# Optimization experiments

Hardware: AMD Instinct MI355X
Metric: run time of the kernel (lower is better)

Reference implementation:

```python
import jax, jax.numpy as jnp
import numpy as np

NUM_CLASSES = 2


def setup_inputs() -> dict:
    key = jax.random.key(0)
    k1, k2, k3 = jax.random.split(key, 3)
    query_features = jax.random.normal(k1, (16384, 2048), dtype=jnp.float32)
    support_features = jax.random.normal(k2, (2048, 2048), dtype=jnp.float32)
    support_labels = jax.random.randint(k3, (2048,), 0, NUM_CLASSES, dtype=jnp.int32)
    return {
        "query_features": query_features,
        "support_features": support_features,
        "support_labels": support_labels,
    }


def _cov(x):
    # unbiased covariance over rows (observations), columns are variables
    xc = x - jnp.mean(x, axis=0, keepdims=True)
    return (xc.T @ xc) / (x.shape[0] - 1)


def _class_stats(features, labels, c):
    # masked per-class mean + unbiased covariance (masked rows contribute 0)
    mask = (labels == c).astype(features.dtype)  # [S]
    n_c = jnp.sum(mask)
    mean_c = (mask @ features) / n_c  # [D]
    xc = (features - mean_c) * mask[:, None]  # [S, D]
    cov_c = (xc.T @ xc) / (n_c - 1.0)  # [D, D]
    return mean_c, cov_c, n_c


def reference(query_features, support_features, support_labels):
    D = support_features.shape[1]
    task_cov = _cov(support_features)  # [D, D]
    eye = jnp.eye(D, dtype=support_features.dtype)

    def per_class(c):
        mean_c, cov_c, n_c = _class_stats(support_features, support_labels, c)
        lam = jnp.minimum(n_c / (n_c + 1.0), 0.1)
        prec = jnp.linalg.inv(lam * cov_c + (1.0 - lam) * task_cov + 0.1 * eye)
        return mean_c, prec

    means, precisions = jax.vmap(per_class)(jnp.arange(NUM_CLASSES))  # [C,D], [C,D,D]

    # Mahalanobis quadratic form: logits[n,c] = -(mu_c - q_n)^T P_c (mu_c - q_n)
    diff = means[:, None, :] - query_features[None, :, :]  # [C, N, D]
    first_half = jnp.einsum("cnd,cde->cne", diff, precisions)  # [C, N, D]
    logits = -jnp.sum(first_half * diff, axis=2).T  # [N, C]
    return logits
```

## Files before the change

kernel.cpp:

```cpp
#include <hip/hip_runtime.h>

#define D   2048
#define S   2048
#define NQ  16384
#define DD  ((long)D * (long)D)

#define IDX_N      0
#define IDX_NORMS  16
#define IDX_S      48
#define IDX_SUM    256
#define IDX_MU     4608
#define IDX_MUF    8704
#define IDX_U      10752
#define IDX_V      14848
#define IDX_W2     18944
#define IDX_ACC    32768
#define SMALL_FLOATS 65536

#define NPOW 8
#define NNS  3

typedef unsigned short u16;
typedef __attribute__((ext_vector_type(8))) short short8;
typedef __attribute__((ext_vector_type(4))) short short4v;
typedef __attribute__((ext_vector_type(4))) float f32x4;

__device__ __forceinline__ u16 f2bf(float f) {
    unsigned u = __float_as_uint(f);
    u += 0x7fff + ((u >> 16) & 1);
    return (u16)(u >> 16);
}

__device__ __forceinline__ float bf2f(u16 b) {
    return __uint_as_float(((unsigned)b) << 16);
}

__device__ __forceinline__ void gl16(const void* g, void* l) {
    __builtin_amdgcn_global_load_lds((const __attribute__((address_space(1))) void*)g,
                                     (__attribute__((address_space(3))) void*)l, 16, 0, 0);
}


__global__ void k_counts(const int* __restrict__ lab, float* __restrict__ W) {
    int c0 = 0, c1 = 0;
    for (int i = threadIdx.x; i < S; i += 256) {
        int l = lab[i];
        c0 += (l == 0);
        c1 += (l == 1);
    }
    atomicAdd(&W[IDX_N + 0], (float)c0);
    atomicAdd(&W[IDX_N + 1], (float)c1);
}

__global__ void k_colsums(const float* __restrict__ X, const int* __restrict__ lab,
                          float* __restrict__ W) {
    int d  = blockIdx.x * 256 + threadIdx.x;
    int i0 = blockIdx.y * 128;
    float s0 = 0.f, s1 = 0.f;
    for (int i = i0; i < i0 + 128; ++i) {
        float v = X[(long)i * D + d];
        int   l = lab[i];
        s0 += (l == 0) ? v : 0.f;
        s1 += (l == 1) ? v : 0.f;
    }
    atomicAdd(&W[IDX_SUM + d],     s0);
    atomicAdd(&W[IDX_SUM + D + d], s1);
}

__global__ void k_stats(float* __restrict__ W) {
    int d = blockIdx.x * 256 + threadIdx.x;
    float n0 = W[IDX_N], n1 = W[IDX_N + 1];
    float s0 = W[IDX_SUM + d], s1 = W[IDX_SUM + D + d];
    W[IDX_MU + d]     = s0 / n0;
    W[IDX_MU + D + d] = s1 / n1;
    W[IDX_MUF + d]    = (s0 + s1) / (float)S;
    unsigned h = (unsigned)d * 2654435761u;
    float r = 0.5f + (float)((h >> 16) & 1023) / 1024.f;
    W[IDX_V + d]     = r;
    W[IDX_V + D + d] = r;
}

__global__ void k_build_M(const float* __restrict__ G, const float* __restrict__ W,
                          u16* __restrict__ Mp) {
    long idx = (long)blockIdx.x * 256 + threadIdx.x;
    int d = (int)(idx / D), e = (int)(idx % D);
    float n0 = W[IDX_N], n1 = W[IDX_N + 1];
    float mufd = W[IDX_MUF + d],     mufe = W[IDX_MUF + e];
    float m0d  = W[IDX_MU + d],      m0e  = W[IDX_MU + e];
    float m1d  = W[IDX_MU + D + d],  m1e  = W[IDX_MU + D + e];
    float a0 = G[idx], a1 = G[DD + idx];
    float task = (a0 + a1 - (float)S * mufd * mufe) * (1.f / (float)(S - 1));
    float c0 = (a0 - n0 * m0d * m0e) / (n0 - 1.f);
    float c1 = (a1 - n1 * m1d * m1e) / (n1 - 1.f);
    float l0 = fminf(n0 / (n0 + 1.f), 0.1f);
    float l1 = fminf(n1 / (n1 + 1.f), 0.1f);
    float eye = (d == e) ? 0.1f : 0.f;
    long po = ((long)(d >> 3) * D + e) * 8 + (d & 7);
    Mp[po]      = f2bf(l0 * c0 + (1.f - l0) * task + eye);
    Mp[DD + po] = f2bf(l1 * c1 + (1.f - l1) * task + eye);
}

__global__ void k_pow(const u16* __restrict__ Mp, float* __restrict__ W, int it) {
    int z = blockIdx.y;
    const u16* Mz = Mp + (long)z * DD;
    float* V  = W + IDX_V  + z * D;
    float* W2 = W + IDX_W2 + z * D;
    const float* in = (it & 1) ? W2 : V;
    float*       out = (it & 1) ? V  : W2;
    float sc = (it > 0) ? rsqrtf(W[IDX_NORMS + z * 16 + it - 1]) : 1.f;
    __shared__ float sin_[D];
    __shared__ float part[8][32];
    for (int e = threadIdx.x; e < D; e += 256) sin_[e] = in[e] * sc;
    __syncthreads();
    int col = blockIdx.x * 32 + (threadIdx.x & 31);
    int sl  = threadIdx.x >> 5;
    float p = 0.f;
    for (int g = sl * 32; g < sl * 32 + 32; ++g) {
        short8 mv = *(const short8*)&Mz[((long)g * D + col) * 8];
#pragma unroll
        for (int j = 0; j < 8; ++j)
            p = fmaf(bf2f((u16)mv[j]), sin_[g * 8 + j], p);
    }
    part[sl][threadIdx.x & 31] = p;
    __syncthreads();
    if (threadIdx.x < 32) {
        float w = 0.f;
#pragma unroll
        for (int s = 0; s < 8; ++s) w += part[s][threadIdx.x];
        out[col] = w;
        float q = w * w;
#pragma unroll
        for (int off = 16; off; off >>= 1) q += __shfl_down(q, off, 32);
        if (threadIdx.x == 0) atomicAdd(&W[IDX_NORMS + z * 16 + it], q);
    }
}

__global__ void k_matvec_u(const u16* __restrict__ Pp, float* __restrict__ W) {
    int z = blockIdx.y;
    const u16* Pz = Pp + (long)z * DD;
    __shared__ float smu[D];
    __shared__ float part[8][32];
    for (int e = threadIdx.x; e < D; e += 256) smu[e] = W[IDX_MU + z * D + e];
    __syncthreads();
    int col = blockIdx.x * 32 + (threadIdx.x & 31);
    int sl  = threadIdx.x >> 5;
    float p = 0.f;
    for (int g = sl * 32; g < sl * 32 + 32; ++g) {
        short8 mv = *(const short8*)&Pz[((long)g * D + col) * 8];
#pragma unroll
        for (int j = 0; j < 8; ++j)
            p = fmaf(bf2f((u16)mv[j]), smu[g * 8 + j], p);
    }
    part[sl][threadIdx.x & 31] = p;
    __syncthreads();
    if (threadIdx.x < 32) {
        float w = 0.f;
#pragma unroll
        for (int s = 0; s < 8; ++s) w += part[s][threadIdx.x];
        W[IDX_U + z * D + col] = w;
    }
}

__global__ void k_dot(float* __restrict__ W) {
    int z = blockIdx.x;
    float t = 0.f;
    for (int d = threadIdx.x; d < D; d += 256)
        t += W[IDX_MU + z * D + d] * W[IDX_U + z * D + d];
    for (int off = 32; off; off >>= 1) t += __shfl_down(t, off);
    __shared__ float sm[4];
    int wv = threadIdx.x >> 6, ln = threadIdx.x & 63;
    if (ln == 0) sm[wv] = t;
    __syncthreads();
    if (threadIdx.x == 0) W[IDX_S + z] = sm[0] + sm[1] + sm[2] + sm[3];
}

__global__ void k_finalize(const float* __restrict__ W, float* __restrict__ out) {
    int idx = blockIdx.x * 256 + threadIdx.x;
    int z = idx & 1;
    out[idx] = -(W[IDX_ACC + idx] + W[IDX_S + z]);
}


__global__ void k_pack_S(const float* __restrict__ Xs, const int* __restrict__ lab,
                         u16* __restrict__ Sp, u16* __restrict__ S01p) {
    int d = blockIdx.x * 256 + threadIdx.x;
    int a = blockIdx.y;
    short8 p, p0, p1;
#pragma unroll
    for (int j = 0; j < 8; ++j) {
        int i = a * 8 + j;
        float v = Xs[(long)i * D + d];
        int   l = lab[i];
        short b = (short)f2bf(v);
        p[j]  = b;
        p0[j] = (l == 0) ? b : (short)0;
        p1[j] = (l == 1) ? b : (short)0;
    }
    long off = ((long)a * D + d) * 8;
    *(short8*)&Sp[off]        = p;
    *(short8*)&S01p[off]      = p0;
    *(short8*)&S01p[DD + off] = p1;
}

#define TLS 520
__global__ void k_pack_Q(const float* __restrict__ Q, u16* __restrict__ Qp) {
    __shared__ u16 tl[32 * TLS];
    int m0 = blockIdx.x * 64;
    int f0 = blockIdx.y * 256;
    int t = threadIdx.x;
#pragma unroll
    for (int p = 0; p < 16; ++p) {
        int idx = p * 256 + t;
        int r  = idx >> 6;
        int c4 = idx & 63;
        float4 v = *(const float4*)&Q[(long)(m0 + r) * D + f0 + c4 * 4];
        u16* dst = &tl[(c4 >> 1) * TLS + r * 8 + (c4 & 1) * 4];
        dst[0] = f2bf(v.x); dst[1] = f2bf(v.y);
        dst[2] = f2bf(v.z); dst[3] = f2bf(v.w);
    }
    __syncthreads();
#pragma unroll
    for (int p = 0; p < 8; ++p) {
        int idx = p * 256 + t;
        int g = idx >> 6;
        int r = idx & 63;
        short8 pk = *(const short8*)&tl[g * TLS + r * 8];
        *(short8*)&Qp[((long)(f0 / 8 + g) * NQ + m0 + r) * 8] = pk;
    }
}

__global__ void __launch_bounds__(512)
bgemmQ(const u16* __restrict__ Ap, const u16* __restrict__ Bp,
       long sA, long sB, int lda, int K,
       const float* __restrict__ u, float* __restrict__ acc2) {
    int z = blockIdx.z;
    const u16* A = Ap + z * sA;
    const u16* B = Bp + z * sB;

    int nwg = gridDim.x * gridDim.y;
    int id  = blockIdx.y * gridDim.x + blockIdx.x;
    int cpx = nwg >> 3;
    int swz = (id & 7) * cpx + (id >> 3);
    int bx = swz % gridDim.x, by = swz / gridDim.x;

    int n0 = bx * 256;
    int m0 = by * 256;
    int tid = threadIdx.x;
    int w = tid >> 6, lane = tid & 63;
    int wr = w >> 2, wc = w & 3;
    int lhi = lane >> 4, llo = lane & 15;

    __shared__ short lds[65536];

    f32x4 acc[8][4];
#pragma unroll
    for (int i = 0; i < 8; ++i)
#pragma unroll
        for (int j = 0; j < 4; ++j) acc[i][j] = (f32x4)(0.f);

    auto stage = [&](int H) {
        char* ldsB = (char*)lds + (H & 3) * 32768;
#pragma unroll
        for (int q = 0; q < 4; ++q) {
            int id4  = w * 4 + q;
            int isB  = id4 >> 4;
            int kg   = (id4 >> 2) & 3;
            int colq = id4 & 3;
            long row = (long)(4 * H + kg);
            const u16* src = isB ? (B + (row * (long)D   + n0 + colq * 64) * 8)
                                 : (A + (row * (long)lda + m0 + colq * 64) * 8);
            gl16((const char*)src + lane * 16,
                 ldsB + isB * 16384 + kg * 4096 + colq * 1024);
        }
    };

    auto compute = [&](int h) {
        const short* As = lds + (h & 3) * 16384 + lhi * 2048;
        const short* Bs = As + 8192;
        short8 af[8], bfr[4];
#pragma unroll
        for (int i = 0; i < 8; ++i)
            af[i] = *(const short8*)&As[(wr * 128 + i * 16 + llo) * 8];
#pragma unroll
        for (int j = 0; j < 4; ++j)
            bfr[j] = *(const short8*)&Bs[(wc * 64 + j * 16 + llo) * 8];
        __builtin_amdgcn_s_setprio(1);
#pragma unroll
        for (int i = 0; i < 8; ++i)
#pragma unroll
            for (int j = 0; j < 4; ++j)
                acc[i][j] = __builtin_amdgcn_mfma_f32_16x16x32_bf16(af[i], bfr[j], acc[i][j], 0, 0, 0);
        __builtin_amdgcn_s_setprio(0);
    };

    const int NH = K >> 5;
    stage(0); stage(1); stage(2);
    for (int h = 0; h <= NH - 3; ++h) {
        asm volatile("s_waitcnt vmcnt(8)" ::: "memory");
        asm volatile("s_barrier" ::: "memory");
        if (h < NH - 3) stage(h + 3);
        compute(h);
    }
    asm volatile("s_waitcnt vmcnt(4)" ::: "memory");
    asm volatile("s_barrier" ::: "memory");
    compute(NH - 2);
    asm volatile("s_waitcnt vmcnt(0)" ::: "memory");
    asm volatile("s_barrier" ::: "memory");
    compute(NH - 1);

    float uv[4];
#pragma unroll
    for (int j = 0; j < 4; ++j) uv[j] = u[z * D + n0 + wc * 64 + j * 16 + llo];
#pragma unroll
    for (int i = 0; i < 8; ++i) {
#pragma unroll
        for (int r = 0; r < 4; ++r) {
            int row = m0 + wr * 128 + i * 16 + lhi * 4 + r;
            float t = 0.f;
#pragma unroll
            for (int j = 0; j < 4; ++j) {
                int n = n0 + wc * 64 + j * 16 + llo;
                float qv = bf2f(A[((long)(n >> 3) * NQ + row) * 8 + (n & 7)]);
                t += (acc[i][j][r] - 2.f * uv[j]) * qv;
            }
            t += __shfl_xor(t, 1);
            t += __shfl_xor(t, 2);
            t += __shfl_xor(t, 4);
            t += __shfl_xor(t, 8);
            if (llo == 0) atomicAdd(&acc2[row * 2 + z], t);
        }
    }
}

template <int EPI>
__global__ void __launch_bounds__(512)
bgemmD(const u16* __restrict__ Ap, const u16* __restrict__ Bp,
       float* __restrict__ Cf, u16* __restrict__ Cp,
       u16* __restrict__ Cp2, const u16* __restrict__ Ep,
       long sA, long sB, long sCf, long sCp,
       int lda, int K,
       const float* __restrict__ u) {
    int z = blockIdx.z;
    const u16* A = Ap + z * sA;
    const u16* B = Bp + z * sB;

    int nwg = gridDim.x * gridDim.y;
    int id  = blockIdx.y * gridDim.x + blockIdx.x;
    int cpx = nwg >> 3;
    int swz = (id & 7) * cpx + (id >> 3);
    int bx = swz % gridDim.x, by = swz / gridDim.x;

    int n0 = bx * 256;
    int m0 = by * 128;
    int tid = threadIdx.x;
    int w = tid >> 6, lane = tid & 63;
    int wr = w >> 2, wc = w & 3;
    int lhi = lane >> 4, llo = lane & 15;

    __shared__ short lds[73728];

    f32x4 acc[4][4];
#pragma unroll
    for (int i = 0; i < 4; ++i)
#pragma unroll
        for (int j = 0; j < 4; ++j) acc[i][j] = (f32x4)(0.f);

    auto stage = [&](int H, int sl) {
        char* ldsB = (char*)lds + sl * 49152;
#pragma unroll
        for (int q = 0; q < 6; ++q) {
            int idq  = w * 6 + q;
            bool isB = idq >= 16;
            int idr  = isB ? idq - 16 : idq;
            int kg   = isB ? (idr >> 2) : (idr >> 1);
            int colq = isB ? (idr & 3)  : (idr & 1);
            long row = (long)(8 * H + kg);
            const u16* src = isB ? (B + (row * (long)D   + n0 + colq * 64) * 8)
                                 : (A + (row * (long)lda + m0 + colq * 64) * 8);
            char* dst = ldsB + (isB ? (16384 + kg * 4096 + colq * 1024)
                                    : (kg * 2048 + colq * 1024));
            gl16((const char*)src + lane * 16, dst);
        }
    };

    auto compute = [&](int h, int sl) {
        const short* slot = lds + sl * 24576;
#pragma unroll
        for (int kk = 0; kk < 2; ++kk) {
            const short* As = slot + (kk * 4 + lhi) * 1024;
            const short* Bs = slot + 8192 + (kk * 4 + lhi) * 2048;
            short8 af[4], bfr[4];
#pragma unroll
            for (int i = 0; i < 4; ++i)
                af[i] = *(const short8*)&As[(wr * 64 + i * 16 + llo) * 8];
#pragma unroll
            for (int j = 0; j < 4; ++j)
                bfr[j] = *(const short8*)&Bs[(wc * 64 + j * 16 + llo) * 8];
            __builtin_amdgcn_s_setprio(1);
#pragma unroll
            for (int i = 0; i < 4; ++i)
#pragma unroll
                for (int j = 0; j < 4; ++j)
                    acc[i][j] = __builtin_amdgcn_mfma_f32_16x16x32_bf16(af[i], bfr[j], acc[i][j], 0, 0, 0);
            __builtin_amdgcn_s_setprio(0);
        }
    };

    const int NH = K >> 6;
    stage(0, 0); stage(1, 1);
    int sl = 0;
    for (int h = 0; h <= NH - 3; ++h) {
        asm volatile("s_waitcnt vmcnt(6)" ::: "memory");
        asm volatile("s_barrier" ::: "memory");
        int sl2 = (sl == 0) ? 2 : sl - 1;
        stage(h + 2, sl2);
        compute(h, sl);
        sl = (sl == 2) ? 0 : sl + 1;
    }
    asm volatile("s_waitcnt vmcnt(6)" ::: "memory");
    asm volatile("s_barrier" ::: "memory");
    compute(NH - 2, sl);
    sl = (sl == 2) ? 0 : sl + 1;
    asm volatile("s_waitcnt vmcnt(0)" ::: "memory");
    asm volatile("s_barrier" ::: "memory");
    compute(NH - 1, sl);

    if (EPI == 0) {
        float* C = Cf + z * sCf;
#pragma unroll
        for (int i = 0; i < 4; ++i) {
            int m_b = m0 + wr * 64 + i * 16 + lhi * 4;
#pragma unroll
            for (int j = 0; j < 4; ++j) {
                int n = n0 + wc * 64 + j * 16 + llo;
#pragma unroll
                for (int r = 0; r < 4; ++r)
                    C[(long)(m_b + r) * D + n] = acc[i][j][r];
            }
        }
    } else if (EPI == 1) {
        u16* P = Cp + z * sCp;
#pragma unroll
        for (int i = 0; i < 4; ++i) {
            int m_b = m0 + wr * 64 + i * 16 + lhi * 4;
#pragma unroll
            for (int j = 0; j < 4; ++j) {
                int n = n0 + wc * 64 + j * 16 + llo;
                short4v pk;
#pragma unroll
                for (int r = 0; r < 4; ++r) {
                    float v = ((m_b + r) == n ? 1.f : 0.f) - acc[i][j][r];
                    pk[r] = (short)f2bf(v);
                }
                *(short4v*)((char*)P + ((long)((m_b >> 3) * D + n)) * 16 + (m_b & 7) * 2) = pk;
            }
        }
    } else if (EPI == 2) {
        u16* P = Cp + z * sCp;
#pragma unroll
        for (int i = 0; i < 4; ++i) {
            int m_b = m0 + wr * 64 + i * 16 + lhi * 4;
#pragma unroll
            for (int j = 0; j < 4; ++j) {
                int n = n0 + wc * 64 + j * 16 + llo;
                long po = ((long)((m_b >> 3) * D + n)) * 16 + (m_b & 7) * 2;
                short4v old = *(const short4v*)((const char*)A + po);
                short4v pk;
#pragma unroll
                for (int r = 0; r < 4; ++r)
                    pk[r] = (short)f2bf(bf2f((u16)old[r]) + acc[i][j][r]);
                *(short4v*)((char*)P + po) = pk;
            }
        }
    } else if (EPI == 5) {
        float lam = sqrtf(u[z * 16 + NPOW - 1]);
        float bb = 1.25f * lam + 0.05f, aa = 0.095f;
        float al = 2.f / (bb - aa);
        float be = -(bb + aa) / (bb - aa);
        float be2 = be * be;
        float t5 = ((16.f * be2 - 20.f) * be2 + 5.f) * be;
        float al2 = al * al, al3 = al2 * al;
        float c4 = -16.f * al3 * al2 / t5;
        float c3 = -80.f * al3 * al * be / t5;
        float c2 = -(160.f * be2 - 20.f) * al3 / t5;
        u16* T = Cp  + z * sCp;
        u16* U = Cp2 + z * DD;
#pragma unroll
        for (int i = 0; i < 4; ++i) {
            int m_b = m0 + wr * 64 + i * 16 + lhi * 4;
#pragma unroll
            for (int j = 0; j < 4; ++j) {
                int n = n0 + wc * 64 + j * 16 + llo;
                long po = ((long)((m_b >> 3) * D + n)) * 16 + (m_b & 7) * 2;
                short4v mv = *(const short4v*)((const char*)A + po);
                short4v tp, up;
#pragma unroll
                for (int r = 0; r < 4; ++r) {
                    float eye = ((m_b + r) == n) ? 1.f : 0.f;
                    float t = acc[i][j][r];
                    tp[r] = (short)f2bf(t);
                    up[r] = (short)f2bf(c2 * eye + c3 * bf2f((u16)mv[r]) + c4 * t);
                }
                *(short4v*)((char*)T + po) = tp;
                *(short4v*)((char*)U + po) = up;
            }
        }
    } else {
        float lam = sqrtf(u[z * 16 + NPOW - 1]);
        float bb = 1.25f * lam + 0.05f, aa = 0.095f;
        float al = 2.f / (bb - aa);
        float be = -(bb + aa) / (bb - aa);
        float be2 = be * be;
        float t5 = ((16.f * be2 - 20.f) * be2 + 5.f) * be;
        float c1 = -(160.f * be2 - 60.f) * al * al * be / t5;
        float c0 = -((80.f * be2 - 60.f) * be2 + 5.f) * al / t5;
        const u16* M = Ep + z * DD;
        u16* P = Cp + z * sCp;
#pragma unroll
        for (int i = 0; i < 4; ++i) {
            int m_b = m0 + wr * 64 + i * 16 + lhi * 4;
#pragma unroll
            for (int j = 0; j < 4; ++j) {
                int n = n0 + wc * 64 + j * 16 + llo;
                long po = ((long)((m_b >> 3) * D + n)) * 16 + (m_b & 7) * 2;
                short4v mv = *(const short4v*)((const char*)M + po);
                short4v pk;
#pragma unroll
                for (int r = 0; r < 4; ++r) {
                    float eye = ((m_b + r) == n) ? 1.f : 0.f;
                    pk[r] = (short)f2bf(acc[i][j][r] + c0 * eye + c1 * bf2f((u16)mv[r]));
                }
                *(short4v*)((char*)P + po) = pk;
            }
        }
    }
}


extern "C" void kernel_launch(void* const* d_in, const int* in_sizes, int n_in,
                              void* d_out, int out_size, void* d_ws, size_t ws_size,
                              hipStream_t stream) {
    const float* Q   = (const float*)d_in[0];
    const float* Xs  = (const float*)d_in[1];
    const int*   lab = (const int*)d_in[2];
    float* out = (float*)d_out;
    float* W   = (float*)d_ws;

    char* BIG = (char*)d_ws + (long)SMALL_FLOATS * 4;
    u16*  Sp   = (u16*)(BIG);
    u16*  S01p = (u16*)(BIG + 8388608L);
    u16*  Rp   = (u16*)(BIG + 25165824L);
    u16*  Mp   = (u16*)(BIG + 41943040L);
    u16*  XpA  = (u16*)(BIG + 58720256L);
    u16*  XpB  = (u16*)(BIG + 75497472L);
    float* F32 = (float*)(BIG + 92274688L);
    u16*  Qp   = (u16*)(BIG);

    hipMemsetAsync(d_ws, 0, SMALL_FLOATS * sizeof(float), stream);

    k_counts<<<1, 256, 0, stream>>>(lab, W);
    k_colsums<<<dim3(D / 256, 16), 256, 0, stream>>>(Xs, lab, W);
    k_stats<<<D / 256, 256, 0, stream>>>(W);
    k_pack_S<<<dim3(D / 256, S / 8), 256, 0, stream>>>(Xs, lab, Sp, S01p);

    bgemmD<0><<<dim3(8, 16, 2), 512, 0, stream>>>(
        S01p, Sp, F32, nullptr, nullptr, nullptr, DD, 0, DD, 0, D, S, nullptr);

    k_build_M<<<(int)(DD / 256), 256, 0, stream>>>(F32, W, Mp);

    for (int it = 0; it < NPOW; ++it)
        k_pow<<<dim3(D / 32, 2), 256, 0, stream>>>(Mp, W, it);

    bgemmD<5><<<dim3(8, 16, 2), 512, 0, stream>>>(
        Mp, Mp, nullptr, Rp, XpB, nullptr, DD, DD, 0, DD, D, D, W + IDX_NORMS);
    bgemmD<6><<<dim3(8, 16, 2), 512, 0, stream>>>(
        Rp, XpB, nullptr, XpA, nullptr, Mp, DD, DD, 0, DD, D, D, W + IDX_NORMS);

    u16* src = XpA;
    for (int it = 0; it < NNS; ++it) {
        u16* dst = (src == XpA) ? XpB : XpA;
        bgemmD<1><<<dim3(8, 16, 2), 512, 0, stream>>>(
            Mp, src, nullptr, Rp, nullptr, nullptr, DD, DD, 0, DD, D, D, nullptr);
        bgemmD<2><<<dim3(8, 16, 2), 512, 0, stream>>>(
            src, Rp, nullptr, dst, nullptr, nullptr, DD, DD, 0, DD, D, D, nullptr);
        src = dst;
    }

    k_matvec_u<<<dim3(D / 32, 2), 256, 0, stream>>>(src, W);
    k_dot<<<2, 256, 0, stream>>>(W);

    k_pack_Q<<<dim3(NQ / 64, D / 256), 256, 0, stream>>>(Q, Qp);

    bgemmQ<<<dim3(8, 64, 2), 512, 0, stream>>>(
        Qp, src, 0, DD, NQ, D, W + IDX_U, W + IDX_ACC);

    k_finalize<<<NQ * 2 / 256, 256, 0, stream>>>(W, out);
}
```

Measured before the change: 847.3 us.

## Shrink bgemmQ tile to 128x256 with 3-slot LDS ring for higher occupancy

```diff
diff --git a/kernel.cpp b/kernel.cpp
--- a/kernel.cpp
+++ b/kernel.cpp
@@ -229,12 +229,11 @@
     }
 }
 
-__global__ void __launch_bounds__(512)
+__global__ void __launch_bounds__(512, 4)
 bgemmQ(const u16* __restrict__ Ap, const u16* __restrict__ Bp,
-       long sA, long sB, int lda, int K,
-       const float* __restrict__ u, float* __restrict__ acc2) {
+       long sB, const float* __restrict__ u, float* __restrict__ acc2) {
     int z = blockIdx.z;
-    const u16* A = Ap + z * sA;
+    const u16* A = Ap;
     const u16* B = Bp + z * sB;
 
     int nwg = gridDim.x * gridDim.y;
@@ -244,78 +243,85 @@
     int bx = swz % gridDim.x, by = swz / gridDim.x;
 
     int n0 = bx * 256;
-    int m0 = by * 256;
+    int m0 = by * 128;
     int tid = threadIdx.x;
     int w = tid >> 6, lane = tid & 63;
-    int wr = w >> 2, wc = w & 3;
+    int wr = (w >> 2) & 1, wc = w & 3;
     int lhi = lane >> 4, llo = lane & 15;
 
-    __shared__ short lds[65536];
-
-    f32x4 acc[8][4];
-#pragma unroll
-    for (int i = 0; i < 8; ++i)
+    __shared__ short lds[36864];
+
+    f32x4 acc[4][4];
+#pragma unroll
+    for (int i = 0; i < 4; ++i)
 #pragma unroll
         for (int j = 0; j < 4; ++j) acc[i][j] = (f32x4)(0.f);
 
-    auto stage = [&](int H) {
-        char* ldsB = (char*)lds + (H & 3) * 32768;
-#pragma unroll
-        for (int q = 0; q < 4; ++q) {
-            int id4  = w * 4 + q;
-            int isB  = id4 >> 4;
-            int kg   = (id4 >> 2) & 3;
-            int colq = id4 & 3;
+    auto stage = [&](int H, int sl) {
+        char* ldsB = (char*)lds + sl * 24576;
+#pragma unroll
+        for (int q = 0; q < 3; ++q) {
+            int idq  = w * 3 + q;
+            bool isB = idq >= 8;
+            int idr  = isB ? idq - 8 : idq;
+            int kg   = isB ? (idr >> 2) : (idr >> 1);
+            int colq = isB ? (idr & 3)  : (idr & 1);
             long row = (long)(4 * H + kg);
-            const u16* src = isB ? (B + (row * (long)D   + n0 + colq * 64) * 8)
-                                 : (A + (row * (long)lda + m0 + colq * 64) * 8);
-            gl16((const char*)src + lane * 16,
-                 ldsB + isB * 16384 + kg * 4096 + colq * 1024);
+            const u16* src = isB ? (B + (row * (long)D  + n0 + colq * 64) * 8)
+                                 : (A + (row * (long)NQ + m0 + colq * 64) * 8);
+            char* dst = ldsB + (isB ? (8192 + kg * 4096 + colq * 1024)
+                                    : (kg * 2048 + colq * 1024));
+            gl16((const char*)src + lane * 16, dst);
         }
     };
 
-    auto compute = [&](int h) {
-        const short* As = lds + (h & 3) * 16384 + lhi * 2048;
-        const short* Bs = As + 8192;
-        short8 af[8], bfr[4];
-#pragma unroll
-        for (int i = 0; i < 8; ++i)
-            af[i] = *(const short8*)&As[(wr * 128 + i * 16 + llo) * 8];
+    auto compute = [&](int h, int sl) {
+        const short* slot = lds + sl * 12288;
+        const short* As = slot + lhi * 1024;
+        const short* Bs = slot + 4096 + lhi * 2048;
+        short8 af[4], bfr[4];
+#pragma unroll
+        for (int i = 0; i < 4; ++i)
+            af[i] = *(const short8*)&As[(wr * 64 + i * 16 + llo) * 8];
 #pragma unroll
         for (int j = 0; j < 4; ++j)
             bfr[j] = *(const short8*)&Bs[(wc * 64 + j * 16 + llo) * 8];
         __builtin_amdgcn_s_setprio(1);
 #pragma unroll
-        for (int i = 0; i < 8; ++i)
+        for (int i = 0; i < 4; ++i)
 #pragma unroll
             for (int j = 0; j < 4; ++j)
                 acc[i][j] = __builtin_amdgcn_mfma_f32_16x16x32_bf16(af[i], bfr[j], acc[i][j], 0, 0, 0);
         __builtin_amdgcn_s_setprio(0);
     };
 
-    const int NH = K >> 5;
-    stage(0); stage(1); stage(2);
+    const int NH = D >> 5;
+    stage(0, 0); stage(1, 1);
+    int sl = 0;
     for (int h = 0; h <= NH - 3; ++h) {
-        asm volatile("s_waitcnt vmcnt(8)" ::: "memory");
+        asm volatile("s_waitcnt vmcnt(3)" ::: "memory");
         asm volatile("s_barrier" ::: "memory");
-        if (h < NH - 3) stage(h + 3);
-        compute(h);
-    }
-    asm volatile("s_waitcnt vmcnt(4)" ::: "memory");
+        int sl2 = (sl == 0) ? 2 : sl - 1;
+        stage(h + 2, sl2);
+        compute(h, sl);
+        sl = (sl == 2) ? 0 : sl + 1;
+    }
+    asm volatile("s_waitcnt vmcnt(3)" ::: "memory");
     asm volatile("s_barrier" ::: "memory");
-    compute(NH - 2);
+    compute(NH - 2, sl);
+    sl = (sl == 2) ? 0 : sl + 1;
     asm volatile("s_waitcnt vmcnt(0)" ::: "memory");
     asm volatile("s_barrier" ::: "memory");
-    compute(NH - 1);
+    compute(NH - 1, sl);
 
     float uv[4];
 #pragma unroll
     for (int j = 0; j < 4; ++j) uv[j] = u[z * D + n0 + wc * 64 + j * 16 + llo];
 #pragma unroll
-    for (int i = 0; i < 8; ++i) {
+    for (int i = 0; i < 4; ++i) {
 #pragma unroll
         for (int r = 0; r < 4; ++r) {
-            int row = m0 + wr * 128 + i * 16 + lhi * 4 + r;
+            int row = m0 + wr * 64 + i * 16 + lhi * 4 + r;
             float t = 0.f;
 #pragma unroll
             for (int j = 0; j < 4; ++j) {
@@ -354,7 +360,7 @@
     int m0 = by * 128;
     int tid = threadIdx.x;
     int w = tid >> 6, lane = tid & 63;
-    int wr = w >> 2, wc = w & 3;
+    int wr = (w >> 2) & 1, wc = w & 3;
     int lhi = lane >> 4, llo = lane & 15;
 
     __shared__ short lds[73728];
@@ -591,8 +597,8 @@
 
     k_pack_Q<<<dim3(NQ / 64, D / 256), 256, 0, stream>>>(Q, Qp);
 
-    bgemmQ<<<dim3(8, 64, 2), 512, 0, stream>>>(
-        Qp, src, 0, DD, NQ, D, W + IDX_U, W + IDX_ACC);
+    bgemmQ<<<dim3(8, NQ / 128, 2), 512, 0, stream>>>(
+        Qp, src, DD, W + IDX_U, W + IDX_ACC);
 
     k_finalize<<<NQ * 2 / 256, 256, 0, stream>>>(W, out);
 }
```

Measured after the change: 836.9 us. No clear change (-1.2%).
